# Optimization experiments

Measured on AMD Instinct MI355X. Metric: run time of the kernel, lower is better.

Reference implementation:

```python
import jax, jax.numpy as jnp
import numpy as np

EPS = 1e-5

def layer_norm(x, gamma, beta):
    mu = jnp.mean(x, axis=-1, keepdims=True)
    var = jnp.var(x, axis=-1, keepdims=True)
    return (x - mu) * jax.lax.rsqrt(var + EPS) * gamma + beta

def setup_inputs() -> dict:
    key = jax.random.key(0)
    ks = jax.random.split(key, 8)
    B, S, D, OUT = 32768, 6, 128, 1024
    return {
        "x": jax.random.normal(ks[0], (B, S, D), dtype=jnp.float32),
        "W_qkv": jax.random.normal(ks[1], (D, 3 * D), dtype=jnp.float32) * 0.02,
        "b_qkv": jnp.zeros((3 * D,), dtype=jnp.float32),
        "g1": jnp.ones((256,), dtype=jnp.float32),
        "be1": jnp.zeros((256,), dtype=jnp.float32),
        "W_fp": jax.random.normal(ks[2], (256, 256), dtype=jnp.float32) * 0.02,
        "b_fp": jnp.zeros((256,), dtype=jnp.float32),
        "g2": jnp.ones((512,), dtype=jnp.float32),
        "be2": jnp.zeros((512,), dtype=jnp.float32),
        "W_s": jax.random.normal(ks[3], (S * 512, OUT), dtype=jnp.float32) * 0.02,
        "b_s": jnp.zeros((OUT,), dtype=jnp.float32),
    }

def reference(x, W_qkv, b_qkv, g1, be1, W_fp, b_fp, g2, be2, W_s, b_s):
    D = 128
    qkv = x @ W_qkv + b_qkv                      # [B,6,384]
    Q, K, V = qkv[..., :D], qkv[..., D:2*D], qkv[..., 2*D:]
    # attention WITHOUT softmax, as in the original module
    attn = jnp.einsum('bqd,bkd->bqk', Q, K)      # [B,6,6]
    attn_result = jnp.einsum('bqk,bkd->bqd', attn, V)  # [B,6,128]
    m = jnp.concatenate([x, attn_result], axis=2)      # [B,6,256]
    n = layer_norm(m, g1, be1)
    n = n @ W_fp + b_fp                          # [B,6,256]
    f = jnp.concatenate([n, m], axis=2)          # [B,6,512]
    f = layer_norm(f, g2, be2)
    f = f.reshape(-1, 6 * 512)                   # [B,3072]
    out = jax.nn.relu(f @ W_s + b_s)             # [B,1024]
    return out
```

## Files before the change

kernel.cpp:

```cpp
#include <hip/hip_runtime.h>
#include <stdint.h>

typedef short bf16x8 __attribute__((ext_vector_type(8)));
typedef float f32x4 __attribute__((ext_vector_type(4)));
typedef uint32_t u32x4 __attribute__((ext_vector_type(4)));
typedef uint32_t u32x2 __attribute__((ext_vector_type(2)));

__device__ __forceinline__ float bf2f(uint16_t b){
  union { uint32_t u; float f; } v; v.u = ((uint32_t)b) << 16; return v.f;
}
__device__ __forceinline__ float u2f(uint32_t u){
  union { uint32_t u; float f; } v; v.u = u; return v.f;
}
__device__ __forceinline__ uint32_t pk_bf16(float a, float b){
  uint32_t r;
  asm("v_cvt_pk_bf16_f32 %0, %1, %2" : "=v"(r) : "v"(a), "v"(b));
  return r;
}
__device__ __forceinline__ uint16_t f2bf(float f){
  return (uint16_t)pk_bf16(f, f);
}

__device__ __forceinline__ void gl2lds16(const uint16_t* g, uint16_t* l) {
  __builtin_amdgcn_global_load_lds((const __attribute__((address_space(1))) void*)g,
                                   (__attribute__((address_space(3))) void*)l, 16, 0, 0);
}

__global__ __launch_bounds__(256) void transpose_cvt(
    const float* __restrict__ src, uint16_t* __restrict__ dst, int K, int N,
    const float* __restrict__ scale)
{
  __shared__ float tile[32][33];
  int n0 = blockIdx.x * 32, k0 = blockIdx.y * 32;
  int tx = threadIdx.x & 31, ty = threadIdx.x >> 5;
  #pragma unroll
  for (int i = 0; i < 4; i++) {
    int k = k0 + ty + 8*i;
    float v = src[(size_t)k * N + n0 + tx];
    if (scale) v *= scale[k];
    tile[ty + 8*i][tx] = v;
  }
  __syncthreads();
  #pragma unroll
  for (int i = 0; i < 4; i++)
    dst[(size_t)(n0 + ty + 8*i) * K + k0 + tx] = f2bf(tile[tx][ty + 8*i]);
}

__global__ __launch_bounds__(256) void fold_fp(
    const float* __restrict__ Wfp, const float* __restrict__ g1,
    const float* __restrict__ be1, const float* __restrict__ bfp,
    float* __restrict__ c1, float* __restrict__ b1p)
{
  int j = threadIdx.x;
  float c = 0.f, b = 0.f;
  for (int k = 0; k < 256; k++) {
    float w = Wfp[k * 256 + j];
    c += g1[k] * w;
    b += be1[k] * w;
  }
  c1[j] = c;
  b1p[j] = b + bfp[j];
}

#define LX 136
#define LQ 392

__global__ __launch_bounds__(512, 4) void fused_mid(
    const float* __restrict__ X, const uint16_t* __restrict__ WqkvT,
    const float* __restrict__ bqkv, const uint16_t* __restrict__ Wfp2T,
    const float* __restrict__ c1, const float* __restrict__ b1p,
    const float* __restrict__ g2, const float* __restrict__ be2,
    uint16_t* __restrict__ F)
{
  __shared__ uint16_t xs[48 * LX];
  __shared__ uint16_t qs[48 * LQ];
  __shared__ float    sb[8 * 36];
  __shared__ float    smu[48], srs[48];
  int t = threadIdx.x;
  int lane = t & 63, wave = t >> 6;
  int lr = lane & 15, lh = lane >> 4;
  size_t r0 = (size_t)blockIdx.x * 48;

  for (int i = t; i < 768; i += 512) {
    int row = i >> 4, c = (i & 15) * 8;
    const float* g = X + (r0 + row) * 128 + c;
    f32x4 v0 = *(const f32x4*)g, v1 = *(const f32x4*)(g + 4);
    u32x4 o;
    o[0] = pk_bf16(v0[0], v0[1]); o[1] = pk_bf16(v0[2], v0[3]);
    o[2] = pk_bf16(v1[0], v1[1]); o[3] = pk_bf16(v1[2], v1[3]);
    *(u32x4*)(xs + row * LX + c) = o;
  }
  __syncthreads();

  {
    f32x4 acc[3][3] = {};
    #pragma unroll
    for (int k0 = 0; k0 < 128; k0 += 32) {
      bf16x8 af[3], bw[3];
      #pragma unroll
      for (int i = 0; i < 3; i++)
        af[i] = *(const bf16x8*)(xs + (i*16 + lr) * LX + k0 + lh*8);
      #pragma unroll
      for (int j = 0; j < 3; j++)
        bw[j] = *(const bf16x8*)(WqkvT + (size_t)(wave*48 + j*16 + lr) * 128 + k0 + lh*8);
      #pragma unroll
      for (int i = 0; i < 3; i++)
        #pragma unroll
        for (int j = 0; j < 3; j++)
          acc[i][j] = __builtin_amdgcn_mfma_f32_16x16x32_bf16(af[i], bw[j], acc[i][j], 0, 0, 0);
    }
    #pragma unroll
    for (int i = 0; i < 3; i++)
      #pragma unroll
      for (int j = 0; j < 3; j++) {
        int col = wave*48 + j*16 + lr;
        float bv = bqkv[col];
        #pragma unroll
        for (int r = 0; r < 4; r++)
          qs[(i*16 + lh*4 + r) * LQ + col] = f2bf(acc[i][j][r] + bv);
      }
  }
  __syncthreads();

  for (int i = t; i < 288; i += 512) {
    int b = i / 36, q = (i / 6) % 6, k = i % 6;
    const uint16_t* Qr = qs + (b*6 + q) * LQ;
    const uint16_t* Kr = qs + (b*6 + k) * LQ + 128;
    float s = 0.f;
    #pragma unroll
    for (int d = 0; d < 16; d++) {
      u32x4 qv = *(const u32x4*)(Qr + d*8);
      u32x4 kv = *(const u32x4*)(Kr + d*8);
      #pragma unroll
      for (int j = 0; j < 4; j++) {
        s += u2f(qv[j] << 16) * u2f(kv[j] << 16)
           + u2f(qv[j] & 0xFFFF0000u) * u2f(kv[j] & 0xFFFF0000u);
      }
    }
    sb[i] = s;
  }
  __syncthreads();

  for (int i = t; i < 1536; i += 512) {
    int r = i >> 5, dp = (i & 31) * 2;
    int b = r / 6;
    const float* sr = sb + b*36 + (r - b*6)*6;
    float a0 = 0.f, a1 = 0.f, a2 = 0.f, a3 = 0.f;
    #pragma unroll
    for (int k = 0; k < 6; k++) {
      u32x2 vu = *(const u32x2*)(qs + (b*6 + k)*LQ + 256 + dp*2);
      float sk = sr[k];
      a0 += sk * u2f(vu[0] << 16);
      a1 += sk * u2f(vu[0] & 0xFFFF0000u);
      a2 += sk * u2f(vu[1] << 16);
      a3 += sk * u2f(vu[1] & 0xFFFF0000u);
    }
    u32x2 o; o[0] = pk_bf16(a0, a1); o[1] = pk_bf16(a2, a3);
    *(u32x2*)((uint32_t*)(qs + r*LQ) + dp) = o;
  }
  __syncthreads();

  if (t < 192) {
    int r = t >> 2, p = t & 3;
    const uint32_t* src = (p < 2) ? (const uint32_t*)(xs + r*LX + p*64)
                                  : (const uint32_t*)(qs + r*LQ + (p - 2)*64);
    float s1 = 0.f, s2 = 0.f;
    #pragma unroll 8
    for (int d = 0; d < 32; d++) {
      uint32_t u = src[d];
      float a = u2f(u << 16), b = u2f(u & 0xFFFF0000u);
      s1 += a + b; s2 += a*a + b*b;
    }
    s1 += __shfl_xor(s1, 1); s2 += __shfl_xor(s2, 1);
    s1 += __shfl_xor(s1, 2); s2 += __shfl_xor(s2, 2);
    float mu = s1 * (1.f/256.f);
    float var = s2 * (1.f/256.f) - mu*mu;
    if (p == 0) { smu[r] = mu; srs[r] = rsqrtf(var + 1e-5f); }
  }
  f32x4 acc2[3][2] = {};
  #pragma unroll
  for (int k0 = 0; k0 < 256; k0 += 32) {
    bf16x8 af[3], bw[2];
    #pragma unroll
    for (int i = 0; i < 3; i++) {
      const uint16_t* mrow = (k0 < 128) ? (xs + (i*16 + lr) * LX + k0)
                                        : (qs + (i*16 + lr) * LQ + (k0 - 128));
      af[i] = *(const bf16x8*)(mrow + lh*8);
    }
    #pragma unroll
    for (int j = 0; j < 2; j++)
      bw[j] = *(const bf16x8*)(Wfp2T + (size_t)(wave*32 + j*16 + lr) * 256 + k0 + lh*8);
    #pragma unroll
    for (int i = 0; i < 3; i++)
      #pragma unroll
      for (int j = 0; j < 2; j++)
        acc2[i][j] = __builtin_amdgcn_mfma_f32_16x16x32_bf16(af[i], bw[j], acc2[i][j], 0, 0, 0);
  }
  __syncthreads();

  #pragma unroll
  for (int i = 0; i < 3; i++)
    #pragma unroll
    for (int j = 0; j < 2; j++) {
      int col = wave*32 + j*16 + lr;
      float c1v = c1[col], b1v = b1p[col];
      #pragma unroll
      for (int r = 0; r < 4; r++) {
        int row = i*16 + lh*4 + r;
        float h = srs[row] * (acc2[i][j][r] - smu[row] * c1v) + b1v;
        qs[row * LQ + 128 + col] = f2bf(h);
      }
    }
  __syncthreads();

  if (t < 192) {
    int r = t >> 2, p = t & 3;
    const uint32_t* src = (p < 2) ? (const uint32_t*)(qs + r*LQ + 128 + p*128)
                        : (p == 2) ? (const uint32_t*)(xs + r*LX)
                                   : (const uint32_t*)(qs + r*LQ);
    float s1 = 0.f, s2 = 0.f;
    #pragma unroll 8
    for (int d = 0; d < 64; d++) {
      uint32_t u = src[d];
      float a = u2f(u << 16), b = u2f(u & 0xFFFF0000u);
      s1 += a + b; s2 += a*a + b*b;
    }
    s1 += __shfl_xor(s1, 1); s2 += __shfl_xor(s2, 1);
    s1 += __shfl_xor(s1, 2); s2 += __shfl_xor(s2, 2);
    float mu = s1 * (1.f/512.f);
    float var = s2 * (1.f/512.f) - mu*mu;
    if (p == 0) { smu[r] = mu; srs[r] = rsqrtf(var + 1e-5f); }
  }
  __syncthreads();

  for (int i = t; i < 3072; i += 512) {
    int r = i >> 6, c0 = (i & 63) * 8;
    float mu = smu[r], rs = srs[r];
    const uint16_t* src = (c0 < 256) ? (qs + r*LQ + 128 + c0)
                        : (c0 < 384) ? (xs + r*LX + (c0 - 256))
                                     : (qs + r*LQ + (c0 - 384));
    bf16x8 v = *(const bf16x8*)src;
    f32x4 gv0 = *(const f32x4*)(g2 + c0), gv1 = *(const f32x4*)(g2 + c0 + 4);
    f32x4 bv0 = *(const f32x4*)(be2 + c0), bv1 = *(const f32x4*)(be2 + c0 + 4);
    float f[8];
    #pragma unroll
    for (int j = 0; j < 4; j++) {
      f[j]   = (bf2f((uint16_t)v[j])   - mu) * rs * gv0[j] + bv0[j];
      f[4+j] = (bf2f((uint16_t)v[4+j]) - mu) * rs * gv1[j] + bv1[j];
    }
    u32x4 o;
    o[0] = pk_bf16(f[0], f[1]); o[1] = pk_bf16(f[2], f[3]);
    o[2] = pk_bf16(f[4], f[5]); o[3] = pk_bf16(f[6], f[7]);
    *(u32x4*)(F + (r0 + r) * 512 + c0) = o;
  }
}

__global__ __launch_bounds__(1024, 4) void out_gemm(
    const uint16_t* __restrict__ F, const uint16_t* __restrict__ WsT,
    const float* __restrict__ b_s, float* __restrict__ OUT)
{
  __shared__ uint16_t lds[2][2][256*64];
  int t = threadIdx.x;
  int lane = t & 63, wave = t >> 6;
  int wm = wave >> 2, wn = wave & 3;
  int lr = lane & 15, lh = lane >> 4;

  int bid = blockIdx.x;
  int swz = (bid & 7) * 64 + (bid >> 3);
  size_t m0 = (size_t)(swz >> 2) * 256;
  int n0 = (swz & 3) * 256;

  int srow = t >> 3;
  int gch  = (t & 7) ^ ((t >> 3) & 7);
  const uint16_t* Ag = F   + (m0 + srow) * 3072 + gch * 8;
  const uint16_t* Bg = WsT + (size_t)(n0 + srow) * 3072 + gch * 8;

#define STAGE(s, tt) do {                                                    \
    int kk0 = (tt) * 64;                                                     \
    uint16_t* la = &lds[s][0][0];                                            \
    uint16_t* lb = &lds[s][1][0];                                            \
    gl2lds16(Ag + kk0,                    la + wave*512);                    \
    gl2lds16(Ag + (size_t)128*3072 + kk0, la + 8192 + wave*512);             \
    gl2lds16(Bg + kk0,                    lb + wave*512);                    \
    gl2lds16(Bg + (size_t)128*3072 + kk0, lb + 8192 + wave*512);             \
  } while(0)

  f32x4 acc[4][4] = {};
  int swlo = lr & 7;

#define COMPUTE(s) do {                                                      \
    const uint16_t* As_ = &lds[s][0][0];                                     \
    const uint16_t* Bs_ = &lds[s][1][0];                                     \
    _Pragma("unroll")                                                        \
    for (int ks = 0; ks < 2; ks++) {                                         \
      int ch = ((ks*4 + lh) ^ swlo) * 8;                                     \
      bf16x8 af[4], bfr[4];                                                  \
      _Pragma("unroll")                                                      \
      for (int i = 0; i < 4; i++)                                            \
        af[i]  = *(const bf16x8*)(As_ + (wm*64 + i*16 + lr)*64 + ch);        \
      _Pragma("unroll")                                                      \
      for (int j = 0; j < 4; j++)                                            \
        bfr[j] = *(const bf16x8*)(Bs_ + (wn*64 + j*16 + lr)*64 + ch);        \
      __builtin_amdgcn_s_setprio(1);                                         \
      _Pragma("unroll")                                                      \
      for (int i = 0; i < 4; i++)                                            \
        _Pragma("unroll")                                                    \
        for (int j = 0; j < 4; j++)                                          \
          acc[i][j] = __builtin_amdgcn_mfma_f32_16x16x32_bf16(af[i], bfr[j], \
                                                              acc[i][j],0,0,0);\
      __builtin_amdgcn_s_setprio(0);                                         \
    }                                                                        \
  } while(0)

  STAGE(0, 0);
  for (int tt = 0; tt < 48; ++tt) {
    int cur = tt & 1;
    asm volatile("s_waitcnt vmcnt(0)" ::: "memory");
    __builtin_amdgcn_s_barrier();
    asm volatile("" ::: "memory");
    if (tt < 47) STAGE(cur ^ 1, tt + 1);
    COMPUTE(cur);
  }

#undef STAGE
#undef COMPUTE

  #pragma unroll
  for (int i = 0; i < 4; i++)
    #pragma unroll
    for (int j = 0; j < 4; j++) {
      int col = n0 + wn*64 + j*16 + lr;
      float bv = b_s[col];
      #pragma unroll
      for (int r = 0; r < 4; r++) {
        size_t row = m0 + wm*64 + i*16 + lh*4 + r;
        OUT[row * 1024 + col] = fmaxf(acc[i][j][r] + bv, 0.f);
      }
    }
}

extern "C" void kernel_launch(void* const* d_in, const int* in_sizes, int n_in,
                              void* d_out, int out_size, void* d_ws, size_t ws_size,
                              hipStream_t stream) {
  const float* x    = (const float*)d_in[0];
  const float* Wqkv = (const float*)d_in[1];
  const float* bqkv = (const float*)d_in[2];
  const float* g1   = (const float*)d_in[3];
  const float* be1  = (const float*)d_in[4];
  const float* Wfp  = (const float*)d_in[5];
  const float* bfp  = (const float*)d_in[6];
  const float* g2   = (const float*)d_in[7];
  const float* be2  = (const float*)d_in[8];
  const float* Ws   = (const float*)d_in[9];
  const float* bs   = (const float*)d_in[10];
  float* out = (float*)d_out;

  uint8_t* ws = (uint8_t*)d_ws;
  uint16_t* F     = (uint16_t*)(ws);
  uint16_t* WqkvT = (uint16_t*)(ws + 201326592ull);
  uint16_t* Wfp2T = (uint16_t*)(ws + 201424896ull);
  uint16_t* WsT   = (uint16_t*)(ws + 201555968ull);
  float*    c1    = (float*)(ws + 207847424ull);
  float*    b1p   = (float*)(ws + 207848448ull);

  transpose_cvt<<<dim3(12, 4), 256, 0, stream>>>(Wqkv, WqkvT, 128, 384, nullptr);
  transpose_cvt<<<dim3(8, 8), 256, 0, stream>>>(Wfp, Wfp2T, 256, 256, g1);
  transpose_cvt<<<dim3(32, 96), 256, 0, stream>>>(Ws, WsT, 3072, 1024, nullptr);
  fold_fp<<<dim3(1), 256, 0, stream>>>(Wfp, g1, be1, bfp, c1, b1p);
  fused_mid<<<dim3(4096), 512, 0, stream>>>(x, WqkvT, bqkv, Wfp2T, c1, b1p,
                                            g2, be2, F);
  out_gemm<<<dim3(512), 1024, 0, stream>>>(F, WsT, bs, out);
}
```

Measured before the change: 397.2 us.

## Fold second LayerNorm affine and mean into output GEMM weights and epilogue

Folds g2 into the transposed W_s during conversion and precomputes per-segment column sums (cgt) and a combined bias (cb). The mid kernel now writes only x*rstd plus a per-row mu*rstd value, and the output GEMM epilogue subtracts a 6-term mean correction. This drops the per-element affine work and the g2/be2 loads from the mid kernel. In exchange it adds a new serial fold kernel over all of W_s, extra epilogue loads and math, and a different rounding profile, since bf16 products no longer cancel the mean before the GEMM.

```diff
diff --git a/kernel.cpp b/kernel.cpp
--- a/kernel.cpp
+++ b/kernel.cpp
@@ -28,7 +28,7 @@
 
 __global__ __launch_bounds__(256) void transpose_cvt(
     const float* __restrict__ src, uint16_t* __restrict__ dst, int K, int N,
-    const float* __restrict__ scale)
+    const float* __restrict__ scale, int smod)
 {
   __shared__ float tile[32][33];
   int n0 = blockIdx.x * 32, k0 = blockIdx.y * 32;
@@ -37,7 +37,7 @@
   for (int i = 0; i < 4; i++) {
     int k = k0 + ty + 8*i;
     float v = src[(size_t)k * N + n0 + tx];
-    if (scale) v *= scale[k];
+    if (scale) v *= scale[k & smod];
     tile[ty + 8*i][tx] = v;
   }
   __syncthreads();
@@ -62,6 +62,26 @@
   b1p[j] = b + bfp[j];
 }
 
+__global__ __launch_bounds__(256) void fold_out(
+    const float* __restrict__ Ws, const float* __restrict__ g2,
+    const float* __restrict__ be2, const float* __restrict__ bs,
+    float* __restrict__ cgt, float* __restrict__ cb)
+{
+  int j = blockIdx.x * 256 + threadIdx.x;
+  float cbv = 0.f;
+  #pragma unroll
+  for (int s = 0; s < 6; s++) {
+    float cg = 0.f;
+    for (int c = 0; c < 512; c++) {
+      float w = Ws[(size_t)(s*512 + c) * 1024 + j];
+      cg  += g2[c] * w;
+      cbv += be2[c] * w;
+    }
+    cgt[s*1024 + j] = cg;
+  }
+  cb[j] = cbv + bs[j];
+}
+
 #define LX 136
 #define LQ 392
 
@@ -69,8 +89,7 @@
     const float* __restrict__ X, const uint16_t* __restrict__ WqkvT,
     const float* __restrict__ bqkv, const uint16_t* __restrict__ Wfp2T,
     const float* __restrict__ c1, const float* __restrict__ b1p,
-    const float* __restrict__ g2, const float* __restrict__ be2,
-    uint16_t* __restrict__ F)
+    uint16_t* __restrict__ Fm, float* __restrict__ rsmu_g)
 {
   __shared__ uint16_t xs[48 * LX];
   __shared__ uint16_t qs[48 * LQ];
@@ -233,31 +252,27 @@
   }
   __syncthreads();
 
+  if (t < 48) rsmu_g[r0 + t] = smu[t] * srs[t];
   for (int i = t; i < 3072; i += 512) {
     int r = i >> 6, c0 = (i & 63) * 8;
-    float mu = smu[r], rs = srs[r];
+    float rs = srs[r];
     const uint16_t* src = (c0 < 256) ? (qs + r*LQ + 128 + c0)
                         : (c0 < 384) ? (xs + r*LX + (c0 - 256))
                                      : (qs + r*LQ + (c0 - 384));
     bf16x8 v = *(const bf16x8*)src;
-    f32x4 gv0 = *(const f32x4*)(g2 + c0), gv1 = *(const f32x4*)(g2 + c0 + 4);
-    f32x4 bv0 = *(const f32x4*)(be2 + c0), bv1 = *(const f32x4*)(be2 + c0 + 4);
-    float f[8];
-    #pragma unroll
-    for (int j = 0; j < 4; j++) {
-      f[j]   = (bf2f((uint16_t)v[j])   - mu) * rs * gv0[j] + bv0[j];
-      f[4+j] = (bf2f((uint16_t)v[4+j]) - mu) * rs * gv1[j] + bv1[j];
-    }
     u32x4 o;
-    o[0] = pk_bf16(f[0], f[1]); o[1] = pk_bf16(f[2], f[3]);
-    o[2] = pk_bf16(f[4], f[5]); o[3] = pk_bf16(f[6], f[7]);
-    *(u32x4*)(F + (r0 + r) * 512 + c0) = o;
+    o[0] = pk_bf16(bf2f((uint16_t)v[0])*rs, bf2f((uint16_t)v[1])*rs);
+    o[1] = pk_bf16(bf2f((uint16_t)v[2])*rs, bf2f((uint16_t)v[3])*rs);
+    o[2] = pk_bf16(bf2f((uint16_t)v[4])*rs, bf2f((uint16_t)v[5])*rs);
+    o[3] = pk_bf16(bf2f((uint16_t)v[6])*rs, bf2f((uint16_t)v[7])*rs);
+    *(u32x4*)(Fm + (r0 + r) * 512 + c0) = o;
   }
 }
 
 __global__ __launch_bounds__(1024, 4) void out_gemm(
     const uint16_t* __restrict__ F, const uint16_t* __restrict__ WsT,
-    const float* __restrict__ b_s, float* __restrict__ OUT)
+    const float* __restrict__ rsmu, const float* __restrict__ cgt,
+    const float* __restrict__ cb, float* __restrict__ OUT)
 {
   __shared__ uint16_t lds[2][2][256*64];
   int t = threadIdx.x;
@@ -325,16 +340,32 @@
 #undef STAGE
 #undef COMPUTE
 
+  float cgv0[4], cgv1[4], cgv2[4], cgv3[4], cgv4[4], cgv5[4], cbv[4];
+  #pragma unroll
+  for (int j = 0; j < 4; j++) {
+    int col = n0 + wn*64 + j*16 + lr;
+    cbv[j]  = cb[col];
+    cgv0[j] = cgt[0*1024 + col];
+    cgv1[j] = cgt[1*1024 + col];
+    cgv2[j] = cgt[2*1024 + col];
+    cgv3[j] = cgt[3*1024 + col];
+    cgv4[j] = cgt[4*1024 + col];
+    cgv5[j] = cgt[5*1024 + col];
+  }
   #pragma unroll
   for (int i = 0; i < 4; i++)
     #pragma unroll
-    for (int j = 0; j < 4; j++) {
-      int col = n0 + wn*64 + j*16 + lr;
-      float bv = b_s[col];
-      #pragma unroll
-      for (int r = 0; r < 4; r++) {
-        size_t row = m0 + wm*64 + i*16 + lh*4 + r;
-        OUT[row * 1024 + col] = fmaxf(acc[i][j][r] + bv, 0.f);
+    for (int r = 0; r < 4; r++) {
+      size_t row = m0 + wm*64 + i*16 + lh*4 + r;
+      const float* rm = rsmu + row * 6;
+      float rm0 = rm[0], rm1 = rm[1], rm2 = rm[2];
+      float rm3 = rm[3], rm4 = rm[4], rm5 = rm[5];
+      #pragma unroll
+      for (int j = 0; j < 4; j++) {
+        int col = n0 + wn*64 + j*16 + lr;
+        float corr = rm0*cgv0[j] + rm1*cgv1[j] + rm2*cgv2[j]
+                   + rm3*cgv3[j] + rm4*cgv4[j] + rm5*cgv5[j];
+        OUT[row * 1024 + col] = fmaxf(acc[i][j][r] - corr + cbv[j], 0.f);
       }
     }
 }
@@ -362,12 +393,16 @@
   uint16_t* WsT   = (uint16_t*)(ws + 201555968ull);
   float*    c1    = (float*)(ws + 207847424ull);
   float*    b1p   = (float*)(ws + 207848448ull);
-
-  transpose_cvt<<<dim3(12, 4), 256, 0, stream>>>(Wqkv, WqkvT, 128, 384, nullptr);
-  transpose_cvt<<<dim3(8, 8), 256, 0, stream>>>(Wfp, Wfp2T, 256, 256, g1);
-  transpose_cvt<<<dim3(32, 96), 256, 0, stream>>>(Ws, WsT, 3072, 1024, nullptr);
+  float*    rsmu  = (float*)(ws + 207849472ull);
+  float*    cgt   = (float*)(ws + 208635904ull);
+  float*    cb    = (float*)(ws + 208660480ull);
+
+  transpose_cvt<<<dim3(12, 4), 256, 0, stream>>>(Wqkv, WqkvT, 128, 384, nullptr, 0);
+  transpose_cvt<<<dim3(8, 8), 256, 0, stream>>>(Wfp, Wfp2T, 256, 256, g1, 255);
+  transpose_cvt<<<dim3(32, 96), 256, 0, stream>>>(Ws, WsT, 3072, 1024, g2, 511);
   fold_fp<<<dim3(1), 256, 0, stream>>>(Wfp, g1, be1, bfp, c1, b1p);
+  fold_out<<<dim3(4), 256, 0, stream>>>(Ws, g2, be2, bs, cgt, cb);
   fused_mid<<<dim3(4096), 512, 0, stream>>>(x, WqkvT, bqkv, Wfp2T, c1, b1p,
-                                            g2, be2, F);
-  out_gemm<<<dim3(512), 1024, 0, stream>>>(F, WsT, bs, out);
-}
+                                            F, rsmu);
+  out_gemm<<<dim3(512), 1024, 0, stream>>>(F, WsT, rsmu, cgt, cb, out);
+}
```

Result: slower. 533.4 us (+34.3%).
